# Kernel optimization log

Hardware: AMD Instinct MI355X
Metric: run time of the kernel (lower is better)

The kernel has to match this reference:

```python
import jax, jax.numpy as jnp
import numpy as np

N_FFT = 64
HOP = 32
PAD = N_FFT // 2

def _window():
    # torch.hann_window(n_fft) is periodic: 0.5*(1 - cos(2*pi*n/N))
    n = jnp.arange(N_FFT, dtype=jnp.float32)
    return 0.5 * (1.0 - jnp.cos(2.0 * jnp.pi * n / N_FFT))

def _frame_idx(n_frames):
    return jnp.arange(n_frames)[:, None] * HOP + jnp.arange(N_FFT)[None, :]

def _stft(x):
    # x: [..., T] -> complex spectrogram [..., n_frames, F] (torch center=True, reflect pad)
    xp = jnp.pad(x, [(0, 0)] * (x.ndim - 1) + [(PAD, PAD)], mode='reflect')
    Tp = xp.shape[-1]
    n_frames = (Tp - N_FFT) // HOP + 1
    frames = xp[..., _frame_idx(n_frames)] * _window()  # [..., n_frames, n_fft]
    return jnp.fft.rfft(frames, axis=-1)

def _istft(spec, T):
    # spec: [..., n_frames, F] -> signal [..., T] (torch istft with length=T)
    w = _window()
    frames = jnp.fft.irfft(spec, n=N_FFT, axis=-1) * w  # [..., n_frames, n_fft]
    n_frames = frames.shape[-2]
    Tp = T + 2 * PAD
    idx = _frame_idx(n_frames)
    ola = jnp.zeros(frames.shape[:-2] + (Tp,), frames.dtype).at[..., idx].add(frames)
    env = jnp.zeros((Tp,), frames.dtype).at[idx].add(w * w)
    env = jnp.where(env > 1e-11, env, 1.0)
    return (ola / env)[..., PAD:PAD + T]

def reference(x, weight):
    # x: [B, C_in, T], weight: [C_out, C_in, F]
    B, C, T = x.shape
    U = _stft(x)  # [B, C_in, n_frames, F] complex
    # Linearity: sum over input channels in frequency domain, then one ISTFT per output channel.
    Yr = jnp.einsum('oif,binf->bonf', weight, U.real)
    Yi = jnp.einsum('oif,binf->bonf', weight, U.imag)
    Y = Yr + 1j * Yi  # [B, C_out, n_frames, F]
    return _istft(Y, T)  # [B, C_out, T]

def setup_inputs() -> dict:
    key = jax.random.key(0)
    k1, k2 = jax.random.split(key)
    B, C_in, C_out, T = 8, 64, 64, 16384
    x = jax.random.normal(k1, (B, C_in, T), dtype=jnp.float32)
    weight = jax.random.normal(k2, (C_out, C_in, N_FFT // 2 + 1), dtype=jnp.float32)
    return {"x": x, "weight": weight}
```

## Files before the change

kernel.cpp:

```cpp
#include <hip/hip_runtime.h>
#include <cstddef>

#define TT 16384
#define NFRAMES 513
#define NFP 520
#define BNP (8 * NFP)
#define PI32 0.09817477042468103870f

typedef unsigned int u32;
typedef unsigned short u16;
typedef __attribute__((ext_vector_type(8))) short bf16x8;
typedef __attribute__((ext_vector_type(4))) float f32x4;

#define TAB_WBF 0
#define TAB_BM  (33 * 64 * 72)
#define TAB_BTA (TAB_BM + 80 * 72)
#define TAB_TOT (TAB_BTA + 64 * 72)
#define TF_EINV 0

__device__ __forceinline__ float b2f(u16 h) {
  union { u32 u; float f; } v; v.u = ((u32)h) << 16; return v.f;
}
__device__ __forceinline__ u16 f2b(float f) {
  union { float f; u32 u; } v; v.f = f;
  const u32 r = v.u + 0x7FFFu + ((v.u >> 16) & 1u);
  return (u16)(r >> 16);
}
__device__ __forceinline__ u32 pack2(float a, float b) {
  return (u32)f2b(a) | ((u32)f2b(b) << 16);
}

__global__ __launch_bounds__(256) void k0_tables(const float* __restrict__ W,
                                                 u16* __restrict__ t16,
                                                 float* __restrict__ tf) {
  const int b = blockIdx.x, tid = threadIdx.x;
  if (b < 33) {
    for (int idx = tid; idx < 64 * 72; idx += 256) {
      const int o = idx / 72, i = idx % 72;
      const float v = (i < 64) ? W[(size_t)(o * 64 + i) * 33 + b] : 0.f;
      t16[TAB_WBF + b * 64 * 72 + idx] = f2b(v);
    }
  } else if (b == 33) {
    for (int idx = tid; idx < 80 * 72; idx += 256) {
      const int fc = idx / 72, j = idx % 72;
      float v = 0.f;
      if (j < 64 && fc < 65) {
        const float wj = 0.5f * (1.0f - cosf((float)j * PI32));
        if (fc < 64) {
          const int f = fc >> 1;
          const float ang = (float)((f * j) & 63) * PI32;
          v = wj * ((fc & 1) ? -sinf(ang) : cosf(ang));
        } else {
          v = (j & 1) ? -wj : wj;
        }
      }
      t16[TAB_BM + idx] = f2b(v);
    }
  } else {
    for (int idx = tid; idx < 64 * 72; idx += 256) {
      const int j = idx / 72, cf = idx % 72;
      float v = 0.f;
      if (cf < 65) {
        const int f = cf >> 1;
        const float wj = 0.5f * (1.0f - cosf((float)j * PI32));
        const float sc = ((f == 0) || (f == 32)) ? 0.015625f : 0.03125f;
        const float ang = (float)((f * j) & 63) * PI32;
        v = wj * sc * ((cf & 1) ? -sinf(ang) : cosf(ang));
      }
      t16[TAB_BTA + idx] = f2b(v);
    }
    if (tid < 32) {
      const float c = cosf((float)tid * PI32);
      tf[TF_EINV + tid] = 2.0f / (1.0f + c * c);
    }
  }
}

__global__ __launch_bounds__(256) void k1_stft(const float* __restrict__ x,
                                               const u16* __restrict__ t16,
                                               u16* __restrict__ U) {
  const int tile = blockIdx.x;
  const int ch   = blockIdx.y;
  const int bz   = blockIdx.z;
  const int tid = threadIdx.x;
  __shared__ __align__(16) u16 Bm[80 * 72];
  __shared__ __align__(16) u16 Awt[2][64 * 72];
  __shared__ __align__(16) u16 Cs[66 * 72];
  __shared__ float xef[2][64];

  for (int k = tid; k < 720; k += 256)
    ((uint4*)Bm)[k] = ((const uint4*)(t16 + TAB_BM))[k];

  if (tile == 8) {
    if (tid < 128) {
      const int c = tid >> 6, j = tid & 63;
      const int t = (j < 32) ? (16352 + j) : (16414 - j);
      xef[c][j] = x[(size_t)((bz + 4 * c) * 64 + ch) * TT + t];
    }
    __syncthreads();
    for (int id = tid; id < 132; id += 256) {
      const int c = id / 66, fc = id % 66;
      float s = 0.f;
#pragma unroll 8
      for (int j = 0; j < 64; ++j)
        s = fmaf(xef[c][j], b2f(Bm[fc * 72 + j]), s);
      U[(size_t)(fc * 64 + ch) * BNP + (bz + 4 * c) * NFP + 512] = f2b(s);
    }
    return;
  }

  const int F0 = tile * 64;
  const int wave = tid >> 6, lane = tid & 63;
  const int n = lane & 15, quad = lane >> 4;

  auto issue = [&](const float* xb, float4* v, float& rf) {
    if (tile == 0) {
      if (tid < 32) rf = xb[32 - tid];
      v[0] = *(const float4*)(xb + 4 * (8 + tid) - 32);
      v[1] = *(const float4*)(xb + 4 * (264 + tid) - 32);
    } else {
      const float* src = xb + 32 * F0 - 32;
      v[0] = *(const float4*)(src + 4 * tid);
      v[1] = *(const float4*)(src + 4 * (tid + 256));
      if (tid < 8) v[2] = *(const float4*)(src + 4 * (tid + 512));
    }
  };
  auto writeA = [&](u16* Aw, const float4* v, float rf) {
    if (tile == 0) {
      if (tid < 32) Aw[tid] = f2b(rf);
#pragma unroll
      for (int q = 0; q < 2; ++q) {
        const int c = 8 + tid + 256 * q;
        const uint2 pk = make_uint2(pack2(v[q].x, v[q].y), pack2(v[q].z, v[q].w));
        const int flb = c >> 3, jj = 4 * (c & 7);
        if (flb < 64) *(uint2*)&Aw[flb * 72 + jj] = pk;
        *(uint2*)&Aw[(flb - 1) * 72 + 32 + jj] = pk;
      }
    } else {
#pragma unroll
      for (int q = 0; q < 3; ++q) {
        if (q == 2 && tid >= 8) continue;
        const int c = tid + 256 * q;
        const uint2 pk = make_uint2(pack2(v[q].x, v[q].y), pack2(v[q].z, v[q].w));
        const int flb = c >> 3, jj = 4 * (c & 7);
        if (flb < 64) *(uint2*)&Aw[flb * 72 + jj] = pk;
        if (flb >= 1) *(uint2*)&Aw[(flb - 1) * 72 + 32 + jj] = pk;
      }
    }
  };

  bf16x8 afm[2], afx[2];

  bf16x8 bfr[4][2];
  auto frag = [&](const u16* Aw) {
#pragma unroll
    for (int nt = 0; nt < 4; ++nt)
#pragma unroll
      for (int ks = 0; ks < 2; ++ks)
        bfr[nt][ks] = *(const bf16x8*)&Aw[(nt * 16 + n) * 72 + ks * 32 + quad * 8];
  };
  auto computeCs = [&]() {
    const int npass = (wave == 0) ? 2 : 1;
    for (int pass = 0; pass < npass; ++pass) {
      const bf16x8* af = pass ? afx : afm;
      const int mt = pass ? 4 : wave;
      f32x4 acc[4];
#pragma unroll
      for (int nt = 0; nt < 4; ++nt) acc[nt] = (f32x4){0.f, 0.f, 0.f, 0.f};
#pragma unroll
      for (int ks = 0; ks < 2; ++ks)
#pragma unroll
        for (int nt = 0; nt < 4; ++nt)
          acc[nt] = __builtin_amdgcn_mfma_f32_16x16x32_bf16(af[ks], bfr[nt][ks],
                                                            acc[nt], 0, 0, 0);
#pragma unroll
      for (int nt = 0; nt < 4; ++nt) {
        const int fl = nt * 16 + n;
#pragma unroll
        for (int r = 0; r < 4; ++r) {
          const int fc = mt * 16 + quad * 4 + r;
          if (fc < 66) Cs[fc * 72 + fl] = f2b(acc[nt][r]);
        }
      }
    }
  };
  auto copyout = [&](int beff) {
    const int bnb = beff * NFP + F0;
    for (int k = tid; k < 528; k += 256) {
      const int fc = k >> 3, part = k & 7;
      *(uint4*)(U + (size_t)(fc * 64 + ch) * BNP + bnb + part * 8) =
          *(const uint4*)&Cs[fc * 72 + part * 8];
    }
  };

  const float* xbA = x + (size_t)(bz * 64 + ch) * TT;
  const float* xbB = x + (size_t)((bz + 4) * 64 + ch) * TT;

  float4 va[3] = {}; float ra = 0.f;
  issue(xbA, va, ra);
  writeA(Awt[0], va, ra);
  __syncthreads();

#pragma unroll
  for (int ks = 0; ks < 2; ++ks)
    afm[ks] = *(const bf16x8*)&Bm[(wave * 16 + n) * 72 + ks * 32 + quad * 8];
  if (wave == 0) {
#pragma unroll
    for (int ks = 0; ks < 2; ++ks)
      afx[ks] = *(const bf16x8*)&Bm[(64 + n) * 72 + ks * 32 + quad * 8];
  }

  frag(Awt[0]);
  float4 vb[3] = {}; float rb = 0.f;
  issue(xbB, vb, rb);
  computeCs();
  __syncthreads();

  copyout(bz);
  writeA(Awt[1], vb, rb);
  __syncthreads();

  frag(Awt[1]);
  computeCs();
  __syncthreads();
  copyout(bz + 4);
}

__global__ __launch_bounds__(256) void k2_mix(const u16* __restrict__ t16,
                                              u16* __restrict__ U) {
  const int f   = blockIdx.y;
  const int bn0 = blockIdx.x * 64;
  const int tid = threadIdx.x;
  __shared__ __align__(16) u16 Ut[2 * 64 * 72];
  __shared__ __align__(16) u16 Wl[64 * 72];

  for (int k = tid; k < 576; k += 256)
    ((uint4*)Wl)[k] = ((const uint4*)(t16 + TAB_WBF + f * 64 * 72))[k];

#pragma unroll
  for (int kk = 0; kk < 4; ++kk) {
    const int id = tid + kk * 256;
    const int c = id >> 9, rem = id & 511;
    const int i = rem >> 3, qc = rem & 7;
    const uint4 raw = *(const uint4*)(U + (size_t)((2 * f + c) * 64 + i) * BNP + bn0 + 8 * qc);
    const int col = (((i >> 3) ^ qc) << 3) + (i & 7);
    u16* base = &Ut[c * 4608 + col];
#pragma unroll
    for (int e = 0; e < 8; ++e) {
      const u32 w = ((const u32*)&raw)[e >> 1];
      base[(8 * qc + e) * 72] = (u16)((e & 1) ? (w >> 16) : (w & 0xFFFFu));
    }
  }
  __syncthreads();

  const int wave = tid >> 6, lane = tid & 63;
  const int n = lane & 15, quad = lane >> 4;
  const int mt = wave;

  bf16x8 af[2];
#pragma unroll
  for (int ks = 0; ks < 2; ++ks)
    af[ks] = *(const bf16x8*)&Wl[(mt * 16 + n) * 72 + ks * 32 + quad * 8];

  f32x4 acc[4][2];
#pragma unroll
  for (int nt = 0; nt < 4; ++nt)
#pragma unroll
    for (int c = 0; c < 2; ++c) acc[nt][c] = (f32x4){0.f, 0.f, 0.f, 0.f};

#pragma unroll
  for (int ks = 0; ks < 2; ++ks)
#pragma unroll
    for (int nt = 0; nt < 4; ++nt) {
      const int q = nt * 16 + n;
      const int chunk = (((ks << 2) + quad) ^ ((q >> 3) & 7)) << 3;
#pragma unroll
      for (int c = 0; c < 2; ++c) {
        const bf16x8 bf = *(const bf16x8*)&Ut[c * 4608 + q * 72 + chunk];
        acc[nt][c] = __builtin_amdgcn_mfma_f32_16x16x32_bf16(af[ks], bf,
                                                             acc[nt][c], 0, 0, 0);
      }
    }
  __syncthreads();

#pragma unroll
  for (int nt = 0; nt < 4; ++nt) {
    const int col = nt * 16 + n;
#pragma unroll
    for (int c = 0; c < 2; ++c)
#pragma unroll
      for (int r = 0; r < 4; ++r) {
        const int o = mt * 16 + quad * 4 + r;
        Ut[(c * 64 + o) * 72 + col] = f2b(acc[nt][c][r]);
      }
  }
  __syncthreads();

  for (int k = tid; k < 1024; k += 256) {
    const int row = k >> 3, part = k & 7;
    const int c = row >> 6, o = row & 63;
    *(uint4*)(U + (size_t)((2 * f + c) * 64 + o) * BNP + bn0 + part * 8) =
        *(const uint4*)&Ut[row * 72 + part * 8];
  }
}

__global__ __launch_bounds__(256, 6) void k3_istft(const u16* __restrict__ Y,
                                                   const u16* __restrict__ t16,
                                                   const float* __restrict__ tf,
                                                   float* __restrict__ out) {
  const int tile = blockIdx.x;
  const int o    = blockIdx.y;
  const int b    = blockIdx.z;
  const int n0 = tile * 64;
  const int tid = threadIdx.x;
  __shared__ __align__(16) u16 BtA[64 * 72];
  __shared__ __align__(16) u16 Yt[80 * 64];
  __shared__ __align__(16) u16 y64[72];
  __shared__ __align__(16) float einv[32];

  for (int k = tid; k < 576; k += 256)
    ((uint4*)BtA)[k] = ((const uint4*)(t16 + TAB_BTA))[k];

  const size_t ybase = (size_t)b * NFP + n0;
  for (int id = tid; id < 576; id += 256) {
    const int cf = id / 9, oct = id % 9;
    const uint4 raw = *(const uint4*)(Y + (size_t)(cf * 64 + o) * BNP + ybase + oct * 8);
    const u16* s = (const u16*)&raw;
#pragma unroll
    for (int e = 0; e < 8; ++e) {
      const int row = oct * 8 + e;
      const int sw = (row ^ (row >> 3)) & 7;
      Yt[row * 64 + ((((cf >> 3) ^ sw) << 3) | (cf & 7))] = s[e];
    }
  }
  if (tid < 9)
    *(uint4*)&y64[tid * 8] =
        *(const uint4*)(Y + (size_t)(64 * 64 + o) * BNP + ybase + tid * 8);
  if (tid < 32) einv[tid] = tf[TF_EINV + tid];
  __syncthreads();

  const int wave = tid >> 6, lane = tid & 63;
  const int n = lane & 15, quad = lane >> 4;

  const int jrowA = wave * 8 + (n & 7) + (n >> 3) * 32;
  bf16x8 af[2];
#pragma unroll
  for (int ks = 0; ks < 2; ++ks)
    af[ks] = *(const bf16x8*)&BtA[jrowA * 72 + ks * 32 + quad * 8];

  float a64v[4];
#pragma unroll
  for (int r = 0; r < 4; ++r) {
    const int c = quad * 4 + r;
    const int j = wave * 8 + (c & 7) + (c >> 3) * 32;
    a64v[r] = b2f(BtA[j * 72 + 64]);
  }

  f32x4 acc[5];
#pragma unroll
  for (int nt = 0; nt < 5; ++nt) acc[nt] = (f32x4){0.f, 0.f, 0.f, 0.f};
#pragma unroll
  for (int nt = 0; nt < 5; ++nt) {
    const int row = nt * 16 + n;
    const int sw = (row ^ (row >> 3)) & 7;
    const u16* yrow = &Yt[row * 64];
#pragma unroll
    for (int ks = 0; ks < 2; ++ks) {
      const bf16x8 bf = *(const bf16x8*)&yrow[((ks * 4 + quad) ^ sw) << 3];
      acc[nt] = __builtin_amdgcn_mfma_f32_16x16x32_bf16(af[ks], bf, acc[nt], 0, 0, 0);
    }
  }

  const int srcl = (((n + 15) & 15) | ((2 | (quad & 1)) << 4)) << 2;
  const float4 ev = *(const float4*)&einv[wave * 8 + (quad & 1) * 4];
  float* pob = out + (size_t)(b * 64 + o) * TT + 32 * n0 + wave * 8 + (quad & 1) * 4;
  float hiPrev[4] = {0.f, 0.f, 0.f, 0.f};
#pragma unroll
  for (int nt = 0; nt < 5; ++nt) {
    const int fl = nt * 16 + n;
    if (nt < 4 || n == 0) {
      const float yv = b2f(y64[fl]);
#pragma unroll
      for (int r = 0; r < 4; ++r) acc[nt][r] = fmaf(yv, a64v[r], acc[nt][r]);
    }
    float cur[4];
#pragma unroll
    for (int r = 0; r < 4; ++r)
      cur[r] = __int_as_float(
          __builtin_amdgcn_ds_bpermute(srcl, __float_as_int(acc[nt][r])));
    if (quad < 2) {
      const bool valid = (nt < 4) ? (fl > 0) : (n == 0);
      if (valid) {
        float v[4];
#pragma unroll
        for (int r = 0; r < 4; ++r)
          v[r] = (acc[nt][r] + ((n == 0) ? hiPrev[r] : cur[r])) * ev[r];
        *(float4*)(pob + (fl - 1) * 32) = make_float4(v[0], v[1], v[2], v[3]);
      }
    }
#pragma unroll
    for (int r = 0; r < 4; ++r) hiPrev[r] = cur[r];
  }
}

extern "C" void kernel_launch(void* const* d_in, const int* in_sizes, int n_in,
                              void* d_out, int out_size, void* d_ws, size_t ws_size,
                              hipStream_t stream) {
  const float* x  = (const float*)d_in[0];
  const float* wt = (const float*)d_in[1];
  float* out = (float*)d_out;
  u16* U = (u16*)d_ws;
  u16* t16 = (u16*)((char*)d_ws + (size_t)66 * 64 * BNP * 2);
  float* tf = (float*)(t16 + TAB_TOT);

  dim3 blk(256);
  k0_tables<<<dim3(35),       blk, 0, stream>>>(wt, t16, tf);
  k1_stft  <<<dim3(9, 64, 4), blk, 0, stream>>>(x, t16, U);
  k2_mix   <<<dim3(65, 33),   blk, 0, stream>>>(t16, U);
  k3_istft <<<dim3(8, 64, 8), blk, 0, stream>>>(U, t16, tf, out);
}
```

Baseline: 135.0 us.

## Process two batches per iSTFT block with prefetched second Y tile

Each k3_istft block now handles two batch indices (bz and bz+4), halving the grid in z. The second batch's Y loads are issued before the first batch's MFMA/OLA compute and scattered into a second LDS buffer afterwards, so global load latency overlaps compute, and the BtA table load is amortized across two batches. Occupancy bound drops from 6 to 4 blocks per CU and LDS and register use grow, which may reduce latency hiding across blocks.

Result: slower. 139.2 us (+3.1%).

```diff
diff --git a/kernel.cpp b/kernel.cpp
--- a/kernel.cpp
+++ b/kernel.cpp
@@ -150,7 +150,6 @@
   };
 
   bf16x8 afm[2], afx[2];
-
   bf16x8 bfr[4][2];
   auto frag = [&](const u16* Aw) {
 #pragma unroll
@@ -304,43 +303,66 @@
   }
 }
 
-__global__ __launch_bounds__(256, 6) void k3_istft(const u16* __restrict__ Y,
+__global__ __launch_bounds__(256, 4) void k3_istft(const u16* __restrict__ Y,
                                                    const u16* __restrict__ t16,
                                                    const float* __restrict__ tf,
                                                    float* __restrict__ out) {
   const int tile = blockIdx.x;
   const int o    = blockIdx.y;
-  const int b    = blockIdx.z;
+  const int bz   = blockIdx.z;
   const int n0 = tile * 64;
   const int tid = threadIdx.x;
   __shared__ __align__(16) u16 BtA[64 * 72];
-  __shared__ __align__(16) u16 Yt[80 * 64];
-  __shared__ __align__(16) u16 y64[72];
+  __shared__ __align__(16) u16 Yt[2][80 * 64];
+  __shared__ __align__(16) u16 y64[2][72];
   __shared__ __align__(16) float einv[32];
 
   for (int k = tid; k < 576; k += 256)
     ((uint4*)BtA)[k] = ((const uint4*)(t16 + TAB_BTA))[k];
-
-  const size_t ybase = (size_t)b * NFP + n0;
-  for (int id = tid; id < 576; id += 256) {
-    const int cf = id / 9, oct = id % 9;
-    const uint4 raw = *(const uint4*)(Y + (size_t)(cf * 64 + o) * BNP + ybase + oct * 8);
-    const u16* s = (const u16*)&raw;
-#pragma unroll
-    for (int e = 0; e < 8; ++e) {
-      const int row = oct * 8 + e;
-      const int sw = (row ^ (row >> 3)) & 7;
-      Yt[row * 64 + ((((cf >> 3) ^ sw) << 3) | (cf & 7))] = s[e];
-    }
-  }
-  if (tid < 9)
-    *(uint4*)&y64[tid * 8] =
-        *(const uint4*)(Y + (size_t)(64 * 64 + o) * BNP + ybase + tid * 8);
   if (tid < 32) einv[tid] = tf[TF_EINV + tid];
-  __syncthreads();
+
+  const size_t ybA = (size_t)bz * NFP + n0;
+  const size_t ybB = (size_t)(bz + 4) * NFP + n0;
+
+  auto issueY = [&](size_t yb, uint4* raw, uint4& r64) {
+#pragma unroll
+    for (int q = 0; q < 3; ++q) {
+      const int id = tid + 256 * q;
+      if (q < 2 || id < 576) {
+        const int cf = id / 9, oct = id % 9;
+        raw[q] = *(const uint4*)(Y + (size_t)(cf * 64 + o) * BNP + yb + oct * 8);
+      }
+    }
+    if (tid < 9)
+      r64 = *(const uint4*)(Y + (size_t)(64 * 64 + o) * BNP + yb + tid * 8);
+  };
+  auto scatterY = [&](int buf, const uint4* raw, const uint4& r64) {
+#pragma unroll
+    for (int q = 0; q < 3; ++q) {
+      const int id = tid + 256 * q;
+      if (q < 2 || id < 576) {
+        const int cf = id / 9, oct = id % 9;
+        const u16* s = (const u16*)&raw[q];
+#pragma unroll
+        for (int e = 0; e < 8; ++e) {
+          const int row = oct * 8 + e;
+          const int sw = (row ^ (row >> 3)) & 7;
+          Yt[buf][row * 64 + ((((cf >> 3) ^ sw) << 3) | (cf & 7))] = s[e];
+        }
+      }
+    }
+    if (tid < 9) *(uint4*)&y64[buf][tid * 8] = r64;
+  };
 
   const int wave = tid >> 6, lane = tid & 63;
   const int n = lane & 15, quad = lane >> 4;
+
+  uint4 rawA[3] = {}; uint4 r64A = {};
+  issueY(ybA, rawA, r64A);
+  scatterY(0, rawA, r64A);
+  uint4 rawB[3] = {}; uint4 r64B = {};
+  issueY(ybB, rawB, r64B);
+  __syncthreads();
 
   const int jrowA = wave * 8 + (n & 7) + (n >> 3) * 32;
   bf16x8 af[2];
@@ -356,51 +378,58 @@
     a64v[r] = b2f(BtA[j * 72 + 64]);
   }
 
-  f32x4 acc[5];
-#pragma unroll
-  for (int nt = 0; nt < 5; ++nt) acc[nt] = (f32x4){0.f, 0.f, 0.f, 0.f};
-#pragma unroll
-  for (int nt = 0; nt < 5; ++nt) {
-    const int row = nt * 16 + n;
-    const int sw = (row ^ (row >> 3)) & 7;
-    const u16* yrow = &Yt[row * 64];
-#pragma unroll
-    for (int ks = 0; ks < 2; ++ks) {
-      const bf16x8 bf = *(const bf16x8*)&yrow[((ks * 4 + quad) ^ sw) << 3];
-      acc[nt] = __builtin_amdgcn_mfma_f32_16x16x32_bf16(af[ks], bf, acc[nt], 0, 0, 0);
-    }
-  }
-
   const int srcl = (((n + 15) & 15) | ((2 | (quad & 1)) << 4)) << 2;
   const float4 ev = *(const float4*)&einv[wave * 8 + (quad & 1) * 4];
-  float* pob = out + (size_t)(b * 64 + o) * TT + 32 * n0 + wave * 8 + (quad & 1) * 4;
-  float hiPrev[4] = {0.f, 0.f, 0.f, 0.f};
-#pragma unroll
-  for (int nt = 0; nt < 5; ++nt) {
-    const int fl = nt * 16 + n;
-    if (nt < 4 || n == 0) {
-      const float yv = b2f(y64[fl]);
-#pragma unroll
-      for (int r = 0; r < 4; ++r) acc[nt][r] = fmaf(yv, a64v[r], acc[nt][r]);
-    }
-    float cur[4];
-#pragma unroll
-    for (int r = 0; r < 4; ++r)
-      cur[r] = __int_as_float(
-          __builtin_amdgcn_ds_bpermute(srcl, __float_as_int(acc[nt][r])));
-    if (quad < 2) {
-      const bool valid = (nt < 4) ? (fl > 0) : (n == 0);
-      if (valid) {
-        float v[4];
-#pragma unroll
-        for (int r = 0; r < 4; ++r)
-          v[r] = (acc[nt][r] + ((n == 0) ? hiPrev[r] : cur[r])) * ev[r];
-        *(float4*)(pob + (fl - 1) * 32) = make_float4(v[0], v[1], v[2], v[3]);
-      }
-    }
-#pragma unroll
-    for (int r = 0; r < 4; ++r) hiPrev[r] = cur[r];
-  }
+
+  auto computeOLA = [&](int buf, int beff) {
+    f32x4 acc[5];
+#pragma unroll
+    for (int nt = 0; nt < 5; ++nt) acc[nt] = (f32x4){0.f, 0.f, 0.f, 0.f};
+#pragma unroll
+    for (int nt = 0; nt < 5; ++nt) {
+      const int row = nt * 16 + n;
+      const int sw = (row ^ (row >> 3)) & 7;
+      const u16* yrow = &Yt[buf][row * 64];
+#pragma unroll
+      for (int ks = 0; ks < 2; ++ks) {
+        const bf16x8 bf = *(const bf16x8*)&yrow[((ks * 4 + quad) ^ sw) << 3];
+        acc[nt] = __builtin_amdgcn_mfma_f32_16x16x32_bf16(af[ks], bf, acc[nt], 0, 0, 0);
+      }
+    }
+    float* pob = out + (size_t)(beff * 64 + o) * TT + 32 * n0 + wave * 8 + (quad & 1) * 4;
+    float hiPrev[4] = {0.f, 0.f, 0.f, 0.f};
+#pragma unroll
+    for (int nt = 0; nt < 5; ++nt) {
+      const int fl = nt * 16 + n;
+      if (nt < 4 || n == 0) {
+        const float yv = b2f(y64[buf][fl]);
+#pragma unroll
+        for (int r = 0; r < 4; ++r) acc[nt][r] = fmaf(yv, a64v[r], acc[nt][r]);
+      }
+      float cur[4];
+#pragma unroll
+      for (int r = 0; r < 4; ++r)
+        cur[r] = __int_as_float(
+            __builtin_amdgcn_ds_bpermute(srcl, __float_as_int(acc[nt][r])));
+      if (quad < 2) {
+        const bool valid = (nt < 4) ? (fl > 0) : (n == 0);
+        if (valid) {
+          float v[4];
+#pragma unroll
+          for (int r = 0; r < 4; ++r)
+            v[r] = (acc[nt][r] + ((n == 0) ? hiPrev[r] : cur[r])) * ev[r];
+          *(float4*)(pob + (fl - 1) * 32) = make_float4(v[0], v[1], v[2], v[3]);
+        }
+      }
+#pragma unroll
+      for (int r = 0; r < 4; ++r) hiPrev[r] = cur[r];
+    }
+  };
+
+  computeOLA(0, bz);
+  scatterY(1, rawB, r64B);
+  __syncthreads();
+  computeOLA(1, bz + 4);
 }
 
 extern "C" void kernel_launch(void* const* d_in, const int* in_sizes, int n_in,
@@ -417,5 +446,5 @@
   k0_tables<<<dim3(35),       blk, 0, stream>>>(wt, t16, tf);
   k1_stft  <<<dim3(9, 64, 4), blk, 0, stream>>>(x, t16, U);
   k2_mix   <<<dim3(65, 33),   blk, 0, stream>>>(t16, U);
-  k3_istft <<<dim3(8, 64, 8), blk, 0, stream>>>(U, t16, tf, out);
-}
+  k3_istft <<<dim3(8, 64, 4), blk, 0, stream>>>(U, t16, tf, out);
+}
```
